# Kernel optimization log

Measured on AMD Instinct MI355X. Metric: run time of the kernel, lower is better.

The kernel has to match this reference:

```python
import jax, jax.numpy as jnp
import numpy as np
from jax import lax

T, H, W, HID, K = 128, 128, 128, 32, 3
DN = ('NCDHW', 'OIDHW', 'NCDHW')


def conv3dc(x, w, b=None, squeeze=False):
    # Conv3dC: 3D conv, kernel KxKxK, 'SAME' padding; return_squeezed drops channel dim
    y = lax.conv_general_dilated(x, w, (1, 1, 1), 'SAME', dimension_numbers=DN)
    if b is not None:
        y = y + b.reshape(1, -1, 1, 1, 1)
    if squeeze:
        y = jnp.squeeze(y, 1)
    return y


def setup_inputs() -> dict:
    key = jax.random.key(0)
    ks = jax.random.split(key, 10)
    X = jax.random.normal(ks[0], (1, T, H, W), dtype=jnp.float32)
    U = jax.random.normal(ks[1], (H * W, 1), dtype=jnp.float32) * 0.01
    V = jax.random.normal(ks[2], (1, T), dtype=jnp.float32) * 0.01
    M = jax.random.uniform(ks[3], (1, 1, T, H, W), dtype=jnp.float32)
    convM_w = jax.random.normal(ks[4], (HID, 1, K, K, K), dtype=jnp.float32) * 0.05
    conv0_w = jax.random.normal(ks[5], (1, HID, K, K, K), dtype=jnp.float32) * 0.05
    conv0_b = jnp.zeros((1,), dtype=jnp.float32)
    conv1_w = jax.random.normal(ks[6], (1, HID, K, K, K), dtype=jnp.float32) * 0.05
    conv2_w = jax.random.normal(ks[7], (HID, 1, K, K, K), dtype=jnp.float32) * 0.05
    conv4_w = jax.random.normal(ks[8], (1, HID, K, K, K), dtype=jnp.float32) * 0.05
    return {
        'X': X, 'U': U, 'V': V, 'M': M,
        'convM_w': convM_w, 'conv0_w': conv0_w, 'conv0_b': conv0_b,
        'conv1_w': conv1_w, 'conv2_w': conv2_w, 'conv4_w': conv4_w,
        'tau_s_raw': jnp.float32(1.0),
        'mask_scaling': jnp.float32(5.0),
        'g': jnp.ones((HID,), dtype=jnp.float32),
        'th': jnp.full((128,), 1.8, dtype=jnp.float32),
        'g2': jnp.ones((H,), dtype=jnp.float32),
        'u_learn2': jnp.ones((5,), dtype=jnp.float32),
        'v_learn2': jnp.ones((5,), dtype=jnp.float32),
    }


def reference(X, U, V, M, convM_w, conv0_w, conv0_b, conv1_w, conv2_w, conv4_w,
              tau_s_raw, mask_scaling, g, th, g2, u_learn2, v_learn2):
    tau_s = jax.nn.softplus(tau_s_raw)
    B, Td, Hd, Wd = X.shape
    Mh = conv3dc(M, convM_w)                                       # [1,HID,T,H,W]
    bg = 1.0 - jax.nn.relu(conv3dc(Mh, conv0_w, conv0_b, squeeze=True))  # [1,T,H,W]
    bg2 = jnp.square(bg)
    # 5-step unrolled rank-1 U/V gradient descent (faithful, incl. raw .view on (HW,T))
    for i in range(5):
        temp = bg2 * (X - jnp.reshape(U @ V, (1, Td, Hd, Wd)))
        temp = temp.reshape(Td, Hd * Wd)
        grad_U = temp.T @ V.T                                      # [HW,1]
        U = U + 1e-05 * u_learn2[i] * grad_U
        grad_V = (temp @ U).reshape(1, Td)                         # [1,T]
        V = V + 1e-05 * v_learn2[i] * grad_V
    L = (U @ V).T.reshape(Td, Hd, Wd)[None]                        # [1,T,H,W]
    fg2 = jnp.square(X - L)
    _X = tau_s * conv3dc((1.0 - conv3dc(Mh, conv1_w)) * fg2[:, None], conv2_w)
    Mtmp = Mh + _X                                                 # [1,HID,T,H,W]
    # soft_l1_reweighted2
    z = Mtmp.reshape(1, HID, Td, Hd * Wd)
    th2 = (th[None, None, :] * g2[None, :, None] * g[:, None, None]).reshape(HID, Hd * Wd)
    z = jnp.sign(z) * jax.nn.relu(jnp.abs(z) - th2[None, :, None, :])
    Mtmp = z.reshape(1, HID, Td, Hd, Wd)
    Mtmp = conv3dc(Mtmp, conv4_w, squeeze=True)                    # [1,T,H,W]
    M_out = jax.nn.sigmoid((Mtmp - 0.5) * mask_scaling)
    return (X, U, V, M_out)
```

## Files before the change

kernel.cpp:

```cpp
#include <hip/hip_runtime.h>
#include <math.h>

#define Tn 128
#define Hn 128
#define Wn 128
#define Cn 32
#define NVOX (Tn*Hn*Wn)

typedef float4 f4;
typedef unsigned short ushort_t;
typedef __attribute__((ext_vector_type(8))) short short8;
typedef __attribute__((ext_vector_type(4))) float f32x4;

__device__ __forceinline__ unsigned bfpack2(float a, float b) {
  unsigned ua = __float_as_uint(a), ub = __float_as_uint(b);
  ua = (ua + 0x7FFFu + ((ua >> 16) & 1u)) >> 16;
  ub = (ub + 0x7FFFu + ((ub >> 16) & 1u)) >> 16;
  return ua | (ub << 16);
}
__device__ __forceinline__ unsigned short bf1(float a) {
  unsigned u = __float_as_uint(a);
  u = (u + 0x7FFFu + ((u >> 16) & 1u)) >> 16;
  return (unsigned short)u;
}
__device__ __forceinline__ float bflo(unsigned p) { return __uint_as_float(p << 16); }
__device__ __forceinline__ float bfhi(unsigned p) { return __uint_as_float(p & 0xFFFF0000u); }
__device__ __forceinline__ float bfs(unsigned short s) { return __uint_as_float((unsigned)s << 16); }

union U4S8 { uint4 u; short8 s; };

__global__ __launch_bounds__(256) void k_convM(
    const float* __restrict__ M, const float* __restrict__ wM,
    uint4* __restrict__ Mh, const float* __restrict__ X,
    f4* __restrict__ outX)
{
  __shared__ float sm[1224];
  const int w0 = blockIdx.x*32, h0 = blockIdx.y*4, t0 = blockIdx.z*4;
  const int tid = threadIdx.x;
  const bool interior = (w0 != 0) && (w0 != 96) && (h0 != 0) && (h0 != 124)
                     && (t0 != 0) && (t0 != 124);
  for (int idx = tid; idx < 1224; idx += 256) {
    int lw = idx % 34, r = idx / 34, lh = r % 6, ld = r / 6;
    int gw = w0 - 1 + lw, gh = h0 - 1 + lh, gt = t0 - 1 + ld;
    float v = 0.f;
    if (interior || ((unsigned)gw < Wn && (unsigned)gh < Hn && (unsigned)gt < Tn))
      v = M[((long)gt*Hn + gh)*Wn + gw];
    sm[idx] = v;
  }
  const int bid = (blockIdx.z*32 + blockIdx.y)*4 + blockIdx.x;
  if (tid < 128) outX[bid*128 + tid] = ((const f4*)X)[bid*128 + tid];
  __syncthreads();

  const int wp = (tid & 15)*2, th = (tid>>4)&3, td = tid>>6;
  float2 m2[27];
  #pragma unroll
  for (int kd = 0; kd < 3; ++kd)
    #pragma unroll
    for (int kh = 0; kh < 3; ++kh) {
      const float* row = &sm[(((td+kd)*6) + (th+kh))*34 + wp];
      float2 a = *(const float2*)row;
      float2 b = *(const float2*)(row + 2);
      int k0 = (kd*3 + kh)*3;
      m2[k0+0] = make_float2(a.x, a.y);
      m2[k0+1] = make_float2(a.y, b.x);
      m2[k0+2] = make_float2(b.x, b.y);
    }
  const long vox = ((long)(t0+td)*Hn + (h0+th))*Wn + (w0+wp);
  uint4* dA = Mh + vox*4;
  uint4* dB = Mh + (vox+1)*4;
  #pragma unroll
  for (int j = 0; j < 4; ++j) {
    float rA[8], rB[8];
    #pragma unroll
    for (int e = 0; e < 8; ++e) {
      const int c = 8*j + e;
      float2 acc = {0.f, 0.f};
      #pragma unroll
      for (int k = 0; k < 27; ++k) {
        float wv = wM[c*27 + k];
        acc.x = fmaf(wv, m2[k].x, acc.x);
        acc.y = fmaf(wv, m2[k].y, acc.y);
      }
      rA[e] = acc.x; rB[e] = acc.y;
    }
    uint4 oA, oB;
    oA.x = bfpack2(rA[0],rA[1]); oA.y = bfpack2(rA[2],rA[3]);
    oA.z = bfpack2(rA[4],rA[5]); oA.w = bfpack2(rA[6],rA[7]);
    oB.x = bfpack2(rB[0],rB[1]); oB.y = bfpack2(rB[2],rB[3]);
    oB.z = bfpack2(rB[4],rB[5]); oB.w = bfpack2(rB[6],rB[7]);
    dA[j] = oA; dB[j] = oB;
  }
}

template<int S>
__device__ __forceinline__ auto& sel3(f32x4 (&a0)[4], f32x4 (&a1)[4], f32x4 (&a2)[4]) {
  if constexpr (S == 0) return a0;
  else if constexpr (S == 1) return a1;
  else return a2;
}

template<int KD>
__device__ __forceinline__ void kd_taps(
    const U4S8 (&A)[6][3], const uint4* sB, int bbase, int bstep,
    f32x4 (&acc)[4])
{
  const f32x4 fz = {0.f,0.f,0.f,0.f};
  #pragma unroll
  for (int kh = 0; kh < 3; ++kh)
    #pragma unroll
    for (int kw = 0; kw < 3; ++kw) {
      const int tap = KD*9 + kh*3 + kw;
      U4S8 b; b.u = sB[tap*bstep + bbase];
      const bool first = (KD == 0) && (kh == 0) && (kw == 0);
      #pragma unroll
      for (int lh = 0; lh < 4; ++lh)
        acc[lh] = __builtin_amdgcn_mfma_f32_16x16x32_bf16(
            A[lh+kh][kw].s, b.s, first ? fz : acc[lh], 0, 0, 0);
    }
}

template<int MODE, int P>
__device__ __forceinline__ void plane_step(
    const uint4* __restrict__ SRC, const uint4* sB,
    int tbase, int h0, int w0v, int lidx, int bbase, int bstep,
    int n, int kg, bool wL, bool wR, float scal,
    ushort_t* __restrict__ outH, float* __restrict__ outF,
    f32x4 (&a0)[4], f32x4 (&a1)[4], f32x4 (&a2)[4])
{
  const int gt = tbase - 1 + P;
  const bool tok = (unsigned)gt < Tn;
  U4S8 A[6][3];
  #pragma unroll
  for (int hr = 0; hr < 6; ++hr) {
    const int gh = h0 - 1 + hr;
    if (tok && (unsigned)gh < Hn) {
      const uint4* rowp = SRC + (((long)gt*Hn + gh)*Wn + (w0v - 1))*4;
      A[hr][0].u = rowp[lidx];
      A[hr][1].u = rowp[lidx + 4];
      A[hr][2].u = rowp[lidx + 8];
    } else {
      A[hr][0].u = (uint4){0u,0u,0u,0u};
      A[hr][1].u = (uint4){0u,0u,0u,0u};
      A[hr][2].u = (uint4){0u,0u,0u,0u};
    }
  }
  if (wL && n == 0) {
    #pragma unroll
    for (int hr = 0; hr < 6; ++hr) A[hr][0].u = (uint4){0u,0u,0u,0u};
  }
  if (wR && n == 15) {
    #pragma unroll
    for (int hr = 0; hr < 6; ++hr) A[hr][2].u = (uint4){0u,0u,0u,0u};
  }
  __builtin_amdgcn_sched_barrier(0);

  constexpr int kdlo = (P > 7) ? (P - 7) : 0;
  constexpr int kdhi = (P < 2) ? P : 2;
  if constexpr (0 >= kdlo && 0 <= kdhi)
    kd_taps<0>(A, sB, bbase, bstep, sel3<(P - 0) % 3>(a0, a1, a2));
  if constexpr (1 >= kdlo && 1 <= kdhi)
    kd_taps<1>(A, sB, bbase, bstep, sel3<(P - 1) % 3>(a0, a1, a2));
  if constexpr (2 >= kdlo && 2 <= kdhi)
    kd_taps<2>(A, sB, bbase, bstep, sel3<(P - 2) % 3>(a0, a1, a2));

  if constexpr (P >= 2) {
    constexpr int TR = P - 2;
    f32x4 (&acc)[4] = sel3<TR % 3>(a0, a1, a2);
    const int tt = tbase + TR;
    if constexpr (MODE == 0) {
      if (n < 2) {
        #pragma unroll
        for (int lh = 0; lh < 4; ++lh) {
          const long vbase = ((long)tt*Hn + (h0+lh))*Wn + w0v + kg*4;
          #pragma unroll
          for (int r = 0; r < 4; ++r) {
            float y = acc[lh][r];
            if (n == 0) { float bg = 1.f - fmaxf(y + scal, 0.f); outH[vbase+r] = bf1(bg*bg); }
            else        { outF[vbase+r] = 1.f - y; }
          }
        }
      }
    } else {
      if (n == 0) {
        #pragma unroll
        for (int lh = 0; lh < 4; ++lh) {
          const long vbase = ((long)tt*Hn + (h0+lh))*Wn + w0v + kg*4;
          #pragma unroll
          for (int r = 0; r < 4; ++r) {
            float y = (acc[lh][r] - 0.5f)*scal;
            outF[vbase+r] = 1.f/(1.f + expf(-y));
          }
        }
      }
    }
  }
}

template<int MODE>
__global__ __launch_bounds__(256, 2) void k_conv_fused(
    const uint4* __restrict__ SRC, const float* __restrict__ wAp,
    const float* __restrict__ wBp, const float* __restrict__ bias_or_ms,
    ushort_t* __restrict__ outH, float* __restrict__ outF)
{
  __shared__ uint4 sB[MODE == 0 ? 220 : 112];
  const int tid = threadIdx.x;
  const int lane = tid & 63;
  const int n = lane & 15, kg = lane >> 4;

  if constexpr (MODE == 0) {
    for (int idx = tid; idx < 220; idx += 256) {
      uint4 v = {0u,0u,0u,0u};
      if (idx < 216) {
        int tap = idx >> 3, col = (idx >> 2) & 1, kgi = idx & 3;
        const float* wp = col ? wBp : wAp;
        v.x = bfpack2(wp[(kgi*8+0)*27+tap], wp[(kgi*8+1)*27+tap]);
        v.y = bfpack2(wp[(kgi*8+2)*27+tap], wp[(kgi*8+3)*27+tap]);
        v.z = bfpack2(wp[(kgi*8+4)*27+tap], wp[(kgi*8+5)*27+tap]);
        v.w = bfpack2(wp[(kgi*8+6)*27+tap], wp[(kgi*8+7)*27+tap]);
      }
      sB[idx] = v;
    }
  } else {
    for (int idx = tid; idx < 112; idx += 256) {
      uint4 v = {0u,0u,0u,0u};
      if (idx < 108) {
        int tap = idx >> 2, kgi = idx & 3;
        v.x = bfpack2(wAp[(kgi*8+0)*27+tap], wAp[(kgi*8+1)*27+tap]);
        v.y = bfpack2(wAp[(kgi*8+2)*27+tap], wAp[(kgi*8+3)*27+tap]);
        v.z = bfpack2(wAp[(kgi*8+4)*27+tap], wAp[(kgi*8+5)*27+tap]);
        v.w = bfpack2(wAp[(kgi*8+6)*27+tap], wAp[(kgi*8+7)*27+tap]);
      }
      sB[idx] = v;
    }
  }
  const float scal = bias_or_ms[0];
  const int bbase = (MODE == 0) ? ((n < 2) ? (n*4 + kg) : (216 + kg))
                                : ((n == 0) ? kg : (108 + kg));
  const int bstep = (MODE == 0) ? ((n < 2) ? 8 : 0) : ((n == 0) ? 4 : 0);

  const int w0v = blockIdx.x*16, h0 = blockIdx.y*4;
  const int wv = __builtin_amdgcn_readfirstlane(tid >> 6);
  const int tbase = (blockIdx.z*4 + wv)*8;
  const int lidx = n*4 + kg;
  const bool wL = (w0v == 0), wR = (w0v == Wn-16);
  __syncthreads();

  f32x4 a0[4], a1[4], a2[4];

  #define PS(P) plane_step<MODE,P>(SRC, sB, tbase, h0, w0v, lidx, bbase, bstep, \
                                   n, kg, wL, wR, scal, outH, outF, a0, a1, a2);
  PS(0) PS(1) PS(2) PS(3) PS(4) PS(5) PS(6) PS(7) PS(8) PS(9)
  #undef PS
}

__global__ __launch_bounds__(512) void k_G(
    const float* __restrict__ X, const ushort_t* __restrict__ bg2h,
    const float* __restrict__ U0, const float* __restrict__ V0,
    float* __restrict__ G)
{
  __shared__ float Vs[128], Ucol[128], red[512];
  const int h = blockIdx.x;
  const int tid = threadIdx.x;
  const int w = tid & 127, tq = tid >> 7;
  if (tid < 128) Vs[tid] = V0[tid];
  else if (tid < 256) Ucol[tid-128] = U0[(tid-128)*128 + h];
  __syncthreads();
  const float vw = Vs[w];
  float acc = 0.f;
  const int tstart = tq*32;
  for (int t = tstart; t < tstart+32; ++t) {
    int idx = (t*Hn + h)*Wn + w;
    acc += bfs(bg2h[idx])*(X[idx] - Ucol[t]*vw)*Vs[t];
  }
  red[tid] = acc;
  __syncthreads();
  if (tq == 0)
    G[h*128 + w] = red[w] + red[128+w] + red[256+w] + red[384+w];
}

__global__ __launch_bounds__(256) void k_dotT(
    const float* __restrict__ X, const ushort_t* __restrict__ bg2h,
    const float* __restrict__ U0, const float* __restrict__ V0,
    const float* __restrict__ D, float* __restrict__ out)
{
  __shared__ float Uc[128], Vs[128], red[256];
  const int t = blockIdx.x, tid = threadIdx.x;
  if (tid < 128) { Uc[tid] = U0[t*128 + tid]; Vs[tid] = V0[tid]; }
  __syncthreads();
  float acc = 0.f;
  for (int idx = tid; idx < 16384; idx += 256) {
    int h = idx >> 7, w = idx & 127;
    int gi = t*16384 + idx;
    acc += bfs(bg2h[gi])*(X[gi] - Uc[h]*Vs[w])*D[idx];
  }
  red[tid] = acc;
  __syncthreads();
  for (int s = 128; s > 0; s >>= 1) {
    if (tid < s) red[tid] += red[tid+s];
    __syncthreads();
  }
  if (tid == 0) out[t] = red[0];
}

__global__ __launch_bounds__(256) void k_final(
    const float* __restrict__ U0, const float* __restrict__ V0,
    const float* __restrict__ G, const float* __restrict__ u1,
    const float* __restrict__ g2, const float* __restrict__ ul,
    const float* __restrict__ vl,
    float* __restrict__ Ua, float* __restrict__ Va,
    float* __restrict__ outU, float* __restrict__ outV)
{
  const int tid = threadIdx.x;
  float A = 0.f, cu1 = 0.f, cg2 = 0.f;
  #pragma unroll
  for (int i = 0; i < 5; ++i) {
    float ai = 1e-5f*ul[i], bi = 1e-5f*vl[i];
    A += ai; cu1 += bi; cg2 += bi*A;
  }
  for (int idx = tid; idx < 16384; idx += 256) {
    float u = U0[idx] + A*G[idx];
    Ua[idx] = u; outU[idx] = u;
  }
  if (tid < 128) {
    float v = V0[tid] + cu1*u1[tid] + cg2*g2[tid];
    Va[tid] = v; outV[tid] = v;
  }
}

__global__ __launch_bounds__(256) void k_z(
    const float* __restrict__ X, const float* __restrict__ c1m,
    const float* __restrict__ Uf, const float* __restrict__ Vf,
    const float* __restrict__ w2, uint4* __restrict__ Mh,
    const float* __restrict__ taup, const float* __restrict__ g,
    const float* __restrict__ g2, const float* __restrict__ th)
{
  __shared__ float sm[1224];
  const int w0 = blockIdx.x*32, h0 = blockIdx.y*4, t0 = blockIdx.z*4;
  const int tid = threadIdx.x;
  const bool interior = (w0 != 0) && (w0 != 96) && (h0 != 0) && (h0 != 124)
                     && (t0 != 0) && (t0 != 124);
  for (int idx = tid; idx < 1224; idx += 256) {
    int lw = idx % 34, r = idx / 34, lh = r % 6, ld = r / 6;
    int gw = w0 - 1 + lw, gh = h0 - 1 + lh, gt = t0 - 1 + ld;
    float qv = 0.f;
    if (interior || ((unsigned)gw < Wn && (unsigned)gh < Hn && (unsigned)gt < Tn)) {
      long gi = ((long)gt*Hn + gh)*Wn + gw;
      float d = X[gi] - Uf[gh*Wn + gw]*Vf[gt];
      qv = c1m[gi]*d*d;
    }
    sm[idx] = qv;
  }
  __syncthreads();

  const float tau_s = log1pf(expf(taup[0]));
  const int wp = (tid & 15)*2, thl = (tid>>4)&3, td = tid>>6;
  float2 m2[27];
  #pragma unroll
  for (int kd = 0; kd < 3; ++kd)
    #pragma unroll
    for (int kh = 0; kh < 3; ++kh) {
      const float* row = &sm[(((td+kd)*6) + (thl+kh))*34 + wp];
      float2 a = *(const float2*)row;
      float2 b = *(const float2*)(row + 2);
      int k0 = (kd*3 + kh)*3;
      m2[k0+0] = make_float2(a.x, a.y);
      m2[k0+1] = make_float2(a.y, b.x);
      m2[k0+2] = make_float2(b.x, b.y);
    }
  const int h = h0 + thl, w = w0 + wp;
  const long vox = ((long)(t0+td)*Hn + h)*Wn + w;
  const float g2h = g2[h];
  const float thwA = g2h*th[w], thwB = g2h*th[w+1];
  uint4* mA = Mh + vox*4;
  uint4* mB = Mh + (vox+1)*4;
  #pragma unroll
  for (int j = 0; j < 4; ++j) {
    uint4 pA = mA[j], pB = mB[j];
    float inA[8] = {bflo(pA.x), bfhi(pA.x), bflo(pA.y), bfhi(pA.y),
                    bflo(pA.z), bfhi(pA.z), bflo(pA.w), bfhi(pA.w)};
    float inB[8] = {bflo(pB.x), bfhi(pB.x), bflo(pB.y), bfhi(pB.y),
                    bflo(pB.z), bfhi(pB.z), bflo(pB.w), bfhi(pB.w)};
    float oA[8], oB[8];
    #pragma unroll
    for (int e = 0; e < 8; ++e) {
      const int c = 8*j + e;
      float2 acc = {0.f, 0.f};
      #pragma unroll
      for (int k = 0; k < 27; ++k) {
        float wv = w2[c*27 + k];
        acc.x = fmaf(wv, m2[k].x, acc.x);
        acc.y = fmaf(wv, m2[k].y, acc.y);
      }
      float gc = g[c];
      float rA = inA[e] + tau_s*acc.x;
      float aA = fabsf(rA) - gc*thwA;
      oA[e] = (aA > 0.f) ? copysignf(aA, rA) : 0.f;
      float rB = inB[e] + tau_s*acc.y;
      float aB = fabsf(rB) - gc*thwB;
      oB[e] = (aB > 0.f) ? copysignf(aB, rB) : 0.f;
    }
    uint4 qA, qB;
    qA.x = bfpack2(oA[0],oA[1]); qA.y = bfpack2(oA[2],oA[3]);
    qA.z = bfpack2(oA[4],oA[5]); qA.w = bfpack2(oA[6],oA[7]);
    qB.x = bfpack2(oB[0],oB[1]); qB.y = bfpack2(oB[2],oB[3]);
    qB.z = bfpack2(oB[4],oB[5]); qB.w = bfpack2(oB[6],oB[7]);
    mA[j] = qA; mB[j] = qB;
  }
}

extern "C" void kernel_launch(void* const* d_in, const int* in_sizes, int n_in,
                              void* d_out, int out_size, void* d_ws, size_t ws_size,
                              hipStream_t stream)
{
  const float* X   = (const float*)d_in[0];
  const float* U0  = (const float*)d_in[1];
  const float* V0  = (const float*)d_in[2];
  const float* M   = (const float*)d_in[3];
  const float* wM  = (const float*)d_in[4];
  const float* w0  = (const float*)d_in[5];
  const float* b0  = (const float*)d_in[6];
  const float* w1  = (const float*)d_in[7];
  const float* w2  = (const float*)d_in[8];
  const float* w4  = (const float*)d_in[9];
  const float* tau = (const float*)d_in[10];
  const float* ms  = (const float*)d_in[11];
  const float* g   = (const float*)d_in[12];
  const float* th  = (const float*)d_in[13];
  const float* g2  = (const float*)d_in[14];
  const float* ul  = (const float*)d_in[15];
  const float* vl  = (const float*)d_in[16];

  float*    c1m  = (float*)d_ws;
  uint4*    Mh   = (uint4*)((char*)d_ws + (size_t)NVOX*4);
  ushort_t* bg2h = (ushort_t*)((char*)Mh + (size_t)NVOX*64);
  float*    Ua   = (float*)((char*)bg2h + (size_t)NVOX*2);
  float*    Va   = Ua + 16384;
  float*    G    = Va + 128;
  float*    u1   = G + 16384;
  float*    g2v  = u1 + 128;

  float* out_f  = (float*)d_out;
  f4*    outX   = (f4*)d_out;
  float* outU   = out_f + NVOX;
  float* outV   = outU + 16384;
  float* outM   = outV + 128;

  k_convM <<<dim3(4,32,32), 256, 0, stream>>>(M, wM, Mh, X, outX);
  k_conv_fused<0><<<dim3(8,32,4), 256, 0, stream>>>(Mh, w0, w1, b0, bg2h, c1m);

  k_G    <<<128, 512, 0, stream>>>(X, bg2h, U0, V0, G);
  k_dotT <<<128, 256, 0, stream>>>(X, bg2h, U0, V0, U0, u1);
  k_dotT <<<128, 256, 0, stream>>>(X, bg2h, U0, V0, G, g2v);
  k_final<<<1, 256, 0, stream>>>(U0, V0, G, u1, g2v, ul, vl, Ua, Va, outU, outV);

  k_z    <<<dim3(4,32,32), 256, 0, stream>>>(X, c1m, Ua, Va, w2, Mh,
                                             tau, g, g2, th);
  k_conv_fused<1><<<dim3(8,32,4), 256, 0, stream>>>(Mh, w4, w4, ms, nullptr, outM);
}
```

Baseline: 440.8 us.

## Double-buffer plane loads in MFMA conv and use packed FMA in convM

Splits the per-plane conv step into a global-load stage and an MFMA/retire stage. Two register buffers let the loads for plane P+1 be issued while the MFMAs for plane P run, hiding global memory latency. The convM kernel also switches to 2-wide vector FMA, so the compiler can emit packed FP32 FMA instructions. The extra A-fragment buffer raises register pressure and may lower occupancy or cause spills.

```diff
diff --git a/kernel.cpp b/kernel.cpp
--- a/kernel.cpp
+++ b/kernel.cpp
@@ -11,6 +11,7 @@
 typedef unsigned short ushort_t;
 typedef __attribute__((ext_vector_type(8))) short short8;
 typedef __attribute__((ext_vector_type(4))) float f32x4;
+typedef __attribute__((ext_vector_type(2))) float f32x2;
 
 __device__ __forceinline__ unsigned bfpack2(float a, float b) {
   unsigned ua = __float_as_uint(a), ub = __float_as_uint(b);
@@ -26,6 +27,11 @@
 __device__ __forceinline__ float bflo(unsigned p) { return __uint_as_float(p << 16); }
 __device__ __forceinline__ float bfhi(unsigned p) { return __uint_as_float(p & 0xFFFF0000u); }
 __device__ __forceinline__ float bfs(unsigned short s) { return __uint_as_float((unsigned)s << 16); }
+
+__device__ __forceinline__ f32x2 pfma(f32x2 a, float b, f32x2 c) {
+  f32x2 bb = {b, b};
+  return __builtin_elementwise_fma(a, bb, c);
+}
 
 union U4S8 { uint4 u; short8 s; };
 
@@ -52,7 +58,7 @@
   __syncthreads();
 
   const int wp = (tid & 15)*2, th = (tid>>4)&3, td = tid>>6;
-  float2 m2[27];
+  f32x2 m2[27];
   #pragma unroll
   for (int kd = 0; kd < 3; ++kd)
     #pragma unroll
@@ -61,9 +67,9 @@
       float2 a = *(const float2*)row;
       float2 b = *(const float2*)(row + 2);
       int k0 = (kd*3 + kh)*3;
-      m2[k0+0] = make_float2(a.x, a.y);
-      m2[k0+1] = make_float2(a.y, b.x);
-      m2[k0+2] = make_float2(b.x, b.y);
+      m2[k0+0] = (f32x2){a.x, a.y};
+      m2[k0+1] = (f32x2){a.y, b.x};
+      m2[k0+2] = (f32x2){b.x, b.y};
     }
   const long vox = ((long)(t0+td)*Hn + (h0+th))*Wn + (w0+wp);
   uint4* dA = Mh + vox*4;
@@ -74,13 +80,10 @@
     #pragma unroll
     for (int e = 0; e < 8; ++e) {
       const int c = 8*j + e;
-      float2 acc = {0.f, 0.f};
+      f32x2 acc = {0.f, 0.f};
       #pragma unroll
-      for (int k = 0; k < 27; ++k) {
-        float wv = wM[c*27 + k];
-        acc.x = fmaf(wv, m2[k].x, acc.x);
-        acc.y = fmaf(wv, m2[k].y, acc.y);
-      }
+      for (int k = 0; k < 27; ++k)
+        acc = pfma(m2[k], wM[c*27 + k], acc);
       rA[e] = acc.x; rB[e] = acc.y;
     }
     uint4 oA, oB;
@@ -99,37 +102,13 @@
   else return a2;
 }
 
-template<int KD>
-__device__ __forceinline__ void kd_taps(
-    const U4S8 (&A)[6][3], const uint4* sB, int bbase, int bstep,
-    f32x4 (&acc)[4])
-{
-  const f32x4 fz = {0.f,0.f,0.f,0.f};
-  #pragma unroll
-  for (int kh = 0; kh < 3; ++kh)
-    #pragma unroll
-    for (int kw = 0; kw < 3; ++kw) {
-      const int tap = KD*9 + kh*3 + kw;
-      U4S8 b; b.u = sB[tap*bstep + bbase];
-      const bool first = (KD == 0) && (kh == 0) && (kw == 0);
-      #pragma unroll
-      for (int lh = 0; lh < 4; ++lh)
-        acc[lh] = __builtin_amdgcn_mfma_f32_16x16x32_bf16(
-            A[lh+kh][kw].s, b.s, first ? fz : acc[lh], 0, 0, 0);
-    }
-}
-
-template<int MODE, int P>
-__device__ __forceinline__ void plane_step(
-    const uint4* __restrict__ SRC, const uint4* sB,
-    int tbase, int h0, int w0v, int lidx, int bbase, int bstep,
-    int n, int kg, bool wL, bool wR, float scal,
-    ushort_t* __restrict__ outH, float* __restrict__ outF,
-    f32x4 (&a0)[4], f32x4 (&a1)[4], f32x4 (&a2)[4])
+template<int P>
+__device__ __forceinline__ void load_plane(
+    const uint4* __restrict__ SRC, int tbase, int h0, int w0v, int lidx,
+    int n, bool wL, bool wR, U4S8 (&A)[6][3])
 {
   const int gt = tbase - 1 + P;
   const bool tok = (unsigned)gt < Tn;
-  U4S8 A[6][3];
   #pragma unroll
   for (int hr = 0; hr < 6; ++hr) {
     const int gh = h0 - 1 + hr;
@@ -152,8 +131,36 @@
     #pragma unroll
     for (int hr = 0; hr < 6; ++hr) A[hr][2].u = (uint4){0u,0u,0u,0u};
   }
-  __builtin_amdgcn_sched_barrier(0);
-
+}
+
+template<int KD>
+__device__ __forceinline__ void kd_taps(
+    const U4S8 (&A)[6][3], const uint4* sB, int bbase, int bstep,
+    f32x4 (&acc)[4])
+{
+  const f32x4 fz = {0.f,0.f,0.f,0.f};
+  #pragma unroll
+  for (int kh = 0; kh < 3; ++kh)
+    #pragma unroll
+    for (int kw = 0; kw < 3; ++kw) {
+      const int tap = KD*9 + kh*3 + kw;
+      U4S8 b; b.u = sB[tap*bstep + bbase];
+      const bool first = (KD == 0) && (kh == 0) && (kw == 0);
+      #pragma unroll
+      for (int lh = 0; lh < 4; ++lh)
+        acc[lh] = __builtin_amdgcn_mfma_f32_16x16x32_bf16(
+            A[lh+kh][kw].s, b.s, first ? fz : acc[lh], 0, 0, 0);
+    }
+}
+
+template<int MODE, int P>
+__device__ __forceinline__ void mfma_retire(
+    const uint4* sB, const U4S8 (&A)[6][3],
+    int tbase, int h0, int w0v, int bbase, int bstep,
+    int n, int kg, float scal,
+    ushort_t* __restrict__ outH, float* __restrict__ outF,
+    f32x4 (&a0)[4], f32x4 (&a1)[4], f32x4 (&a2)[4])
+{
   constexpr int kdlo = (P > 7) ? (P - 7) : 0;
   constexpr int kdhi = (P < 2) ? P : 2;
   if constexpr (0 >= kdlo && 0 <= kdhi)
@@ -246,11 +253,28 @@
   __syncthreads();
 
   f32x4 a0[4], a1[4], a2[4];
-
-  #define PS(P) plane_step<MODE,P>(SRC, sB, tbase, h0, w0v, lidx, bbase, bstep, \
-                                   n, kg, wL, wR, scal, outH, outF, a0, a1, a2);
-  PS(0) PS(1) PS(2) PS(3) PS(4) PS(5) PS(6) PS(7) PS(8) PS(9)
-  #undef PS
+  U4S8 Aa[6][3], Ab[6][3];
+
+  #define PL(P, AR) load_plane<P>(SRC, tbase, h0, w0v, lidx, n, wL, wR, AR);
+  #define PM(P, AR) mfma_retire<MODE,P>(sB, AR, tbase, h0, w0v, bbase, bstep, \
+                                        n, kg, scal, outH, outF, a0, a1, a2);
+  #define SB __builtin_amdgcn_sched_barrier(0);
+
+  PL(0, Aa) PL(1, Ab) SB
+  PM(0, Aa) PL(2, Aa) SB
+  PM(1, Ab) PL(3, Ab) SB
+  PM(2, Aa) PL(4, Aa) SB
+  PM(3, Ab) PL(5, Ab) SB
+  PM(4, Aa) PL(6, Aa) SB
+  PM(5, Ab) PL(7, Ab) SB
+  PM(6, Aa) PL(8, Aa) SB
+  PM(7, Ab) PL(9, Ab) SB
+  PM(8, Aa) SB
+  PM(9, Ab)
+
+  #undef PL
+  #undef PM
+  #undef SB
 }
 
 __global__ __launch_bounds__(512) void k_G(
```

Result: no change. 443.3 us (+0.6%).
